# Performance work log

Measured on AMD Instinct MI355X. Metric: run time of the kernel, lower is better.

The kernel has to match this reference:

```python
import jax, jax.numpy as jnp
import numpy as np

A = 64            # n_agent == n_enemy == n_ally
MOVE = 4          # move_direction
ES = 5            # enemy_shape
ALS = 5           # ally_shape
NACT = 6          # n_actions
D = ES + ALS + NACT   # 16, transformer token dim
OBS = MOVE + ES * A + (ALS + NACT + A) * A  # 5124
B = 256


def setup_inputs() -> dict:
    key = jax.random.key(0)
    ks = jax.random.split(key, 5)
    s = 1.0 / np.sqrt(D)
    return {
        "inputs": jax.random.normal(ks[0], (B, A, OBS), dtype=jnp.float32),
        "Wq": jax.random.normal(ks[1], (D, D), dtype=jnp.float32) * s,
        "bq": jnp.zeros((D,), dtype=jnp.float32),
        "Wk": jax.random.normal(ks[2], (D, D), dtype=jnp.float32) * s,
        "bk": jnp.zeros((D,), dtype=jnp.float32),
        "Wv": jax.random.normal(ks[3], (D, D), dtype=jnp.float32) * s,
        "bv": jnp.zeros((D,), dtype=jnp.float32),
        "Wo": jax.random.normal(ks[4], (D, D), dtype=jnp.float32) * s,
        "bo": jnp.zeros((D,), dtype=jnp.float32),
    }


def reference(inputs, Wq, bq, Wk, bk, Wv, bv, Wo, bo):
    # dyn slice: skip move dirs, take enemy+ally blocks, reshape per agent,
    # keep first D=16 features of each agent row (drop the A-dim one-hot tail).
    dyn = inputs[:, :, MOVE: MOVE + ES * A + (ALS + NACT + A) * A]
    dyn = dyn.reshape(B, A, A, ES + ALS + NACT + A)[..., :D]  # [B, Ai, Atok, D]

    # single-head self-attention applied independently per (batch, agent i)
    q = dyn @ Wq + bq                                          # [B, Ai, Atok, D]
    k = dyn @ Wk + bk
    v = dyn @ Wv + bv
    scores = jnp.einsum('bitd,bisd->bits', q, k) / jnp.sqrt(jnp.float32(D))
    attn = jax.nn.softmax(scores, axis=-1)                      # [B, Ai, Atok, Atok]
    o = jnp.einsum('bits,bisd->bitd', attn, v) @ Wo + bo        # [B, Ai, Atok, D]

    # relu then sum over agent index i (the outer python loop's accumulation)
    x_sum = jax.nn.relu(o).sum(axis=1)                          # [B, Atok=A, D]

    return jnp.concatenate([inputs[:, :, :MOVE], x_sum], axis=2)  # [B, A, MOVE+D]
```

## Files before the change

kernel.cpp:

```cpp
#include <hip/hip_runtime.h>

#define NA 64
#define MOVE 4
#define OBS 5124
#define ROWS 80
#define NB 256
#define NTASK (NB * NA)
#define OUTC 20
#define WPB 8
#define NPART 8

#define WS_WQ 0
#define WS_WK 64
#define WS_WV 128
#define WS_BK 768
#define WS_BVO 784
#define WS_PART 1024

typedef __attribute__((ext_vector_type(8))) short bf16x8;
typedef __attribute__((ext_vector_type(4))) float f32x4;

__device__ __forceinline__ short f2bf(float f) {
    __bf16 h = (__bf16)f;
    return __builtin_bit_cast(short, h);
}
__device__ __forceinline__ bf16x8 mkfrag4(float a, float b, float c, float d) {
    bf16x8 t;
    t[0] = f2bf(a); t[1] = f2bf(b); t[2] = f2bf(c); t[3] = f2bf(d);
    t[4] = 0; t[5] = 0; t[6] = 0; t[7] = 0;
    return t;
}
__device__ __forceinline__ bf16x8 mkfrag8(f32x4 lo, f32x4 hi) {
    bf16x8 t;
    t[0] = f2bf(lo[0]); t[1] = f2bf(lo[1]); t[2] = f2bf(lo[2]); t[3] = f2bf(lo[3]);
    t[4] = f2bf(hi[0]); t[5] = f2bf(hi[1]); t[6] = f2bf(hi[2]); t[7] = f2bf(hi[3]);
    return t;
}

__global__ __launch_bounds__(256) void prep_kernel(
    const float* __restrict__ Wq,
    const float* __restrict__ Wk, const float* __restrict__ bk,
    const float* __restrict__ Wv, const float* __restrict__ bv,
    const float* __restrict__ Wo, const float* __restrict__ bo,
    float* __restrict__ ws)
{
    __shared__ float sWvo[256];
    const float SC = 0.36067376022224085f;
    int tid = threadIdx.x;
    {
        int e = tid >> 4, d = tid & 15;
        float acc = 0.f;
        #pragma unroll
        for (int c = 0; c < 16; ++c) acc += Wv[e * 16 + c] * Wo[c * 16 + d];
        sWvo[e * 16 + d] = acc;
    }
    __syncthreads();
    if (tid < 64) {
        int g = tid >> 4, c = tid & 15;
        bf16x8 q, k, v;
        #pragma unroll
        for (int r = 0; r < 4; ++r) {
            q[r] = f2bf(Wq[(4 * g + r) * 16 + c]);
            k[r] = f2bf(SC * Wk[(4 * g + r) * 16 + c]);
            v[r] = f2bf(sWvo[(4 * g + r) * 16 + c]);
        }
        #pragma unroll
        for (int r = 4; r < 8; ++r) { q[r] = 0; k[r] = 0; v[r] = 0; }
        ((bf16x8*)ws)[WS_WQ + tid] = q;
        ((bf16x8*)ws)[WS_WK + tid] = k;
        ((bf16x8*)ws)[WS_WV + tid] = v;
    }
    if (tid < 16) {
        ws[WS_BK + tid] = SC * bk[tid];
        float bb = bo[tid];
        #pragma unroll
        for (int c = 0; c < 16; ++c) bb += bv[c] * Wo[c * 16 + tid];
        ws[WS_BVO + tid] = bb;
    }
}

__global__ __launch_bounds__(512, 4) void attn_kernel(
    const float* __restrict__ inp,
    const float* __restrict__ bq,
    float* __restrict__ ws,
    float* __restrict__ out)
{
    __shared__ float sRed[WPB * 64 * OUTC];

    const int tid  = threadIdx.x;
    const int lane = tid & 63;
    const int w    = tid >> 6;
    const int idx  = blockIdx.x * WPB + w;
    const int g    = lane >> 4;
    const int c    = lane & 15;

    const bf16x8 wq = ((const bf16x8*)ws)[WS_WQ + lane];
    const bf16x8 wk = ((const bf16x8*)ws)[WS_WK + lane];
    const bf16x8 wv = ((const bf16x8*)ws)[WS_WV + lane];
    const float4 bq_r  = *(const float4*)(bq + 4 * g);
    const float4 bk_r  = *(const float4*)(ws + WS_BK + 4 * g);
    const float4 bvo_r = *(const float4*)(ws + WS_BVO + 4 * g);

    if (lane == 0) {
        float4 mv = *(const float4*)(inp + (size_t)idx * OBS);
        *(float4*)(out + (size_t)idx * OUTC) = mv;
    }

    const float* dynp = inp + (size_t)idx * OBS + MOVE;
    bf16x8 dy[4];
    #pragma unroll
    for (int i = 0; i < 4; ++i) {
        f32x4 f = __builtin_nontemporal_load(
            (const f32x4*)(dynp + (16 * i + c) * ROWS + 4 * g));
        dy[i] = mkfrag4(f[0], f[1], f[2], f[3]);
    }

    const f32x4 zc = {0.f, 0.f, 0.f, 0.f};

    bf16x8 qb[4], kb[4];
    f32x4 vC[4];
    #pragma unroll
    for (int i = 0; i < 4; ++i) {
        f32x4 qT = __builtin_amdgcn_mfma_f32_16x16x32_bf16(wq, dy[i], zc, 0, 0, 0);
        f32x4 kT = __builtin_amdgcn_mfma_f32_16x16x32_bf16(wk, dy[i], zc, 0, 0, 0);
        vC[i]    = __builtin_amdgcn_mfma_f32_16x16x32_bf16(dy[i], wv, zc, 0, 0, 0);
        qb[i] = mkfrag4(qT[0] + bq_r.x, qT[1] + bq_r.y, qT[2] + bq_r.z, qT[3] + bq_r.w);
        kb[i] = mkfrag4(kT[0] + bk_r.x, kT[1] + bk_r.y, kT[2] + bk_r.z, kT[3] + bk_r.w);
    }
    const bf16x8 vb_lo = mkfrag8(vC[0], vC[1]);
    const bf16x8 vb_hi = mkfrag8(vC[2], vC[3]);

    #pragma unroll
    for (int j = 0; j < 4; ++j) {
        f32x4 s0 = __builtin_amdgcn_mfma_f32_16x16x32_bf16(kb[0], qb[j], zc, 0, 0, 0);
        f32x4 s1 = __builtin_amdgcn_mfma_f32_16x16x32_bf16(kb[1], qb[j], zc, 0, 0, 0);
        f32x4 s2 = __builtin_amdgcn_mfma_f32_16x16x32_bf16(kb[2], qb[j], zc, 0, 0, 0);
        f32x4 s3 = __builtin_amdgcn_mfma_f32_16x16x32_bf16(kb[3], qb[j], zc, 0, 0, 0);

        float part = 0.f;
        #pragma unroll
        for (int r = 0; r < 4; ++r) {
            s0[r] = __builtin_amdgcn_exp2f(s0[r]); part += s0[r];
            s1[r] = __builtin_amdgcn_exp2f(s1[r]); part += s1[r];
            s2[r] = __builtin_amdgcn_exp2f(s2[r]); part += s2[r];
            s3[r] = __builtin_amdgcn_exp2f(s3[r]); part += s3[r];
        }
        part += __shfl_xor(part, 16);
        part += __shfl_xor(part, 32);
        float inv = __builtin_amdgcn_rcpf(part);

        bf16x8 p_lo = mkfrag8(s0, s1);
        bf16x8 p_hi = mkfrag8(s2, s3);

        f32x4 ot;
        ot = __builtin_amdgcn_mfma_f32_16x16x32_bf16(vb_lo, p_lo, zc, 0, 0, 0);
        ot = __builtin_amdgcn_mfma_f32_16x16x32_bf16(vb_hi, p_hi, ot, 0, 0, 0);

        float4 st;
        st.x = fmaxf(fmaf(ot[0], inv, bvo_r.x), 0.f);
        st.y = fmaxf(fmaf(ot[1], inv, bvo_r.y), 0.f);
        st.z = fmaxf(fmaf(ot[2], inv, bvo_r.z), 0.f);
        st.w = fmaxf(fmaf(ot[3], inv, bvo_r.w), 0.f);
        *(float4*)(&sRed[(w * 64 + 16 * j + c) * OUTC + 4 * g]) = st;
    }

    __syncthreads();

    if (tid < 256) {
        int t = tid >> 2, dq = tid & 3;
        float4 st = make_float4(0.f, 0.f, 0.f, 0.f);
        #pragma unroll
        for (int ww = 0; ww < WPB; ++ww) {
            const float4 a = *(const float4*)(&sRed[(ww * 64 + t) * OUTC + dq * 4]);
            st.x += a.x; st.y += a.y; st.z += a.z; st.w += a.w;
        }
        *(float4*)(ws + WS_PART + (size_t)blockIdx.x * 1024 + t * 16 + dq * 4) = st;
    }
}

__global__ __launch_bounds__(256) void reduce_kernel(
    const float* __restrict__ ws, float* __restrict__ out)
{
    const int b   = blockIdx.x;
    const int tid = threadIdx.x;
    const float* pb = ws + WS_PART + (size_t)b * (NPART * 1024);

    int e4 = tid * 4;
    float4 s = make_float4(0.f, 0.f, 0.f, 0.f);
    #pragma unroll
    for (int p = 0; p < NPART; ++p) {
        const float4 a = *(const float4*)(pb + p * 1024 + e4);
        s.x += a.x; s.y += a.y; s.z += a.z; s.w += a.w;
    }
    int t = e4 >> 4, d = e4 & 15;
    *(float4*)(out + ((size_t)b * NA + t) * OUTC + MOVE + d) = s;
}

extern "C" void kernel_launch(void* const* d_in, const int* in_sizes, int n_in,
                              void* d_out, int out_size, void* d_ws, size_t ws_size,
                              hipStream_t stream) {
    const float* inp = (const float*)d_in[0];
    const float* Wq  = (const float*)d_in[1];
    const float* bq  = (const float*)d_in[2];
    const float* Wk  = (const float*)d_in[3];
    const float* bk  = (const float*)d_in[4];
    const float* Wv  = (const float*)d_in[5];
    const float* bv  = (const float*)d_in[6];
    const float* Wo  = (const float*)d_in[7];
    const float* bo  = (const float*)d_in[8];
    float* out = (float*)d_out;
    float* ws  = (float*)d_ws;

    hipLaunchKernelGGL(prep_kernel, dim3(1), dim3(256), 0, stream, Wq, Wk, bk, Wv, bv, Wo, bo, ws);
    hipLaunchKernelGGL(attn_kernel, dim3(NTASK / WPB), dim3(512), 0, stream, inp, bq, ws, out);
    hipLaunchKernelGGL(reduce_kernel, dim3(NB), dim3(256), 0, stream, ws, out);
}
```

Before: 46.39 us.

## Fold Q/K biases into MFMA, stage dyn tile in LDS, shrink blocks to four waves

The Q and K biases are folded into the weight fragments through an extra constant-one column in the input fragment, so the per-element bias adds after each projection disappear. Each wave now loads its 64x16 input tile into shared memory and re-reads it for each projection, which shortens register live ranges, and the weight fragments are loaded only inside the scope where they are used. Blocks drop from 8 to 4 waves with a higher occupancy hint, which doubles the number of partial sums the reduce kernel must combine. This adds LDS traffic and more partial-sum writes in exchange for lower register pressure and higher occupancy.

```diff
diff --git a/kernel.cpp b/kernel.cpp
--- a/kernel.cpp
+++ b/kernel.cpp
@@ -7,13 +7,12 @@
 #define NB 256
 #define NTASK (NB * NA)
 #define OUTC 20
-#define WPB 8
-#define NPART 8
+#define WPB 4
+#define NPART 16
 
 #define WS_WQ 0
 #define WS_WK 64
 #define WS_WV 128
-#define WS_BK 768
 #define WS_BVO 784
 #define WS_PART 1024
 
@@ -24,21 +23,27 @@
     __bf16 h = (__bf16)f;
     return __builtin_bit_cast(short, h);
 }
-__device__ __forceinline__ bf16x8 mkfrag4(float a, float b, float c, float d) {
+__device__ __forceinline__ bf16x8 pack4(f32x4 v) {
     bf16x8 t;
-    t[0] = f2bf(a); t[1] = f2bf(b); t[2] = f2bf(c); t[3] = f2bf(d);
+    t[0] = f2bf(v[0]); t[1] = f2bf(v[1]); t[2] = f2bf(v[2]); t[3] = f2bf(v[3]);
     t[4] = 0; t[5] = 0; t[6] = 0; t[7] = 0;
     return t;
 }
-__device__ __forceinline__ bf16x8 mkfrag8(f32x4 lo, f32x4 hi) {
+__device__ __forceinline__ bf16x8 pack8(f32x4 lo, f32x4 hi) {
     bf16x8 t;
     t[0] = f2bf(lo[0]); t[1] = f2bf(lo[1]); t[2] = f2bf(lo[2]); t[3] = f2bf(lo[3]);
     t[4] = f2bf(hi[0]); t[5] = f2bf(hi[1]); t[6] = f2bf(hi[2]); t[7] = f2bf(hi[3]);
     return t;
 }
+__device__ __forceinline__ bf16x8 dyfrag(f32x4 v, short s4) {
+    bf16x8 t;
+    t[0] = f2bf(v[0]); t[1] = f2bf(v[1]); t[2] = f2bf(v[2]); t[3] = f2bf(v[3]);
+    t[4] = s4; t[5] = 0; t[6] = 0; t[7] = 0;
+    return t;
+}
 
 __global__ __launch_bounds__(256) void prep_kernel(
-    const float* __restrict__ Wq,
+    const float* __restrict__ Wq, const float* __restrict__ bq,
     const float* __restrict__ Wk, const float* __restrict__ bk,
     const float* __restrict__ Wv, const float* __restrict__ bv,
     const float* __restrict__ Wo, const float* __restrict__ bo,
@@ -63,15 +68,15 @@
             q[r] = f2bf(Wq[(4 * g + r) * 16 + c]);
             k[r] = f2bf(SC * Wk[(4 * g + r) * 16 + c]);
             v[r] = f2bf(sWvo[(4 * g + r) * 16 + c]);
-        }
-        #pragma unroll
-        for (int r = 4; r < 8; ++r) { q[r] = 0; k[r] = 0; v[r] = 0; }
+            q[4 + r] = (c == 0) ? f2bf(bq[4 * g + r]) : (short)0;
+            k[4 + r] = (c == 0) ? f2bf(SC * bk[4 * g + r]) : (short)0;
+            v[4 + r] = 0;
+        }
         ((bf16x8*)ws)[WS_WQ + tid] = q;
         ((bf16x8*)ws)[WS_WK + tid] = k;
         ((bf16x8*)ws)[WS_WV + tid] = v;
     }
     if (tid < 16) {
-        ws[WS_BK + tid] = SC * bk[tid];
         float bb = bo[tid];
         #pragma unroll
         for (int c = 0; c < 16; ++c) bb += bv[c] * Wo[c * 16 + tid];
@@ -79,13 +84,12 @@
     }
 }
 
-__global__ __launch_bounds__(512, 4) void attn_kernel(
+__global__ __launch_bounds__(256, 8) void attn_kernel(
     const float* __restrict__ inp,
-    const float* __restrict__ bq,
-    float* __restrict__ ws,
+    const float* __restrict__ ws,
     float* __restrict__ out)
 {
-    __shared__ float sRed[WPB * 64 * OUTC];
+    __shared__ float sBuf[WPB * 1024];
 
     const int tid  = threadIdx.x;
     const int lane = tid & 63;
@@ -93,64 +97,90 @@
     const int idx  = blockIdx.x * WPB + w;
     const int g    = lane >> 4;
     const int c    = lane & 15;
-
-    const bf16x8 wq = ((const bf16x8*)ws)[WS_WQ + lane];
-    const bf16x8 wk = ((const bf16x8*)ws)[WS_WK + lane];
-    const bf16x8 wv = ((const bf16x8*)ws)[WS_WV + lane];
-    const float4 bq_r  = *(const float4*)(bq + 4 * g);
-    const float4 bk_r  = *(const float4*)(ws + WS_BK + 4 * g);
-    const float4 bvo_r = *(const float4*)(ws + WS_BVO + 4 * g);
+    float* chunk = sBuf + (w << 10);
 
     if (lane == 0) {
         float4 mv = *(const float4*)(inp + (size_t)idx * OBS);
         *(float4*)(out + (size_t)idx * OUTC) = mv;
     }
 
-    const float* dynp = inp + (size_t)idx * OBS + MOVE;
-    bf16x8 dy[4];
-    #pragma unroll
-    for (int i = 0; i < 4; ++i) {
-        f32x4 f = __builtin_nontemporal_load(
-            (const f32x4*)(dynp + (16 * i + c) * ROWS + 4 * g));
-        dy[i] = mkfrag4(f[0], f[1], f[2], f[3]);
+    {
+        const float* dynp = inp + (size_t)idx * OBS + MOVE + (size_t)c * ROWS + 4 * g;
+        f32x4 t0 = *(const f32x4*)(dynp + 0 * 16 * ROWS);
+        f32x4 t1 = *(const f32x4*)(dynp + 1 * 16 * ROWS);
+        f32x4 t2 = *(const f32x4*)(dynp + 2 * 16 * ROWS);
+        f32x4 t3 = *(const f32x4*)(dynp + 3 * 16 * ROWS);
+        *(f32x4*)(chunk + (16 * 0 + c) * 16 + 4 * g) = t0;
+        *(f32x4*)(chunk + (16 * 1 + c) * 16 + 4 * g) = t1;
+        *(f32x4*)(chunk + (16 * 2 + c) * 16 + 4 * g) = t2;
+        *(f32x4*)(chunk + (16 * 3 + c) * 16 + 4 * g) = t3;
     }
 
     const f32x4 zc = {0.f, 0.f, 0.f, 0.f};
-
-    bf16x8 qb[4], kb[4];
-    f32x4 vC[4];
-    #pragma unroll
-    for (int i = 0; i < 4; ++i) {
-        f32x4 qT = __builtin_amdgcn_mfma_f32_16x16x32_bf16(wq, dy[i], zc, 0, 0, 0);
-        f32x4 kT = __builtin_amdgcn_mfma_f32_16x16x32_bf16(wk, dy[i], zc, 0, 0, 0);
-        vC[i]    = __builtin_amdgcn_mfma_f32_16x16x32_bf16(dy[i], wv, zc, 0, 0, 0);
-        qb[i] = mkfrag4(qT[0] + bq_r.x, qT[1] + bq_r.y, qT[2] + bq_r.z, qT[3] + bq_r.w);
-        kb[i] = mkfrag4(kT[0] + bk_r.x, kT[1] + bk_r.y, kT[2] + bk_r.z, kT[3] + bk_r.w);
-    }
-    const bf16x8 vb_lo = mkfrag8(vC[0], vC[1]);
-    const bf16x8 vb_hi = mkfrag8(vC[2], vC[3]);
+    const short s4 = (g == 0) ? (short)0x3f80 : (short)0;
+    const float4 bvo_r = *(const float4*)(ws + WS_BVO + 4 * g);
+
+    bf16x8 qb[4], kb[4], vb_lo, vb_hi;
+    {
+        const bf16x8 wq = ((const bf16x8*)ws)[WS_WQ + lane];
+        #pragma unroll
+        for (int i = 0; i < 4; ++i) {
+            f32x4 d = *(const f32x4*)(chunk + i * 256 + c * 16 + 4 * g);
+            qb[i] = pack4(__builtin_amdgcn_mfma_f32_16x16x32_bf16(wq, dyfrag(d, s4), zc, 0, 0, 0));
+        }
+    }
+    {
+        const bf16x8 wk = ((const bf16x8*)ws)[WS_WK + lane];
+        #pragma unroll
+        for (int i = 0; i < 4; ++i) {
+            f32x4 d = *(const f32x4*)(chunk + i * 256 + c * 16 + 4 * g);
+            kb[i] = pack4(__builtin_amdgcn_mfma_f32_16x16x32_bf16(wk, dyfrag(d, s4), zc, 0, 0, 0));
+        }
+    }
+    {
+        const bf16x8 wv = ((const bf16x8*)ws)[WS_WV + lane];
+        f32x4 v0, v1, v2, v3;
+        {
+            f32x4 d = *(const f32x4*)(chunk + 0 * 256 + c * 16 + 4 * g);
+            v0 = __builtin_amdgcn_mfma_f32_16x16x32_bf16(dyfrag(d, s4), wv, zc, 0, 0, 0);
+            d = *(const f32x4*)(chunk + 1 * 256 + c * 16 + 4 * g);
+            v1 = __builtin_amdgcn_mfma_f32_16x16x32_bf16(dyfrag(d, s4), wv, zc, 0, 0, 0);
+            d = *(const f32x4*)(chunk + 2 * 256 + c * 16 + 4 * g);
+            v2 = __builtin_amdgcn_mfma_f32_16x16x32_bf16(dyfrag(d, s4), wv, zc, 0, 0, 0);
+            d = *(const f32x4*)(chunk + 3 * 256 + c * 16 + 4 * g);
+            v3 = __builtin_amdgcn_mfma_f32_16x16x32_bf16(dyfrag(d, s4), wv, zc, 0, 0, 0);
+        }
+        vb_lo = pack8(v0, v1);
+        vb_hi = pack8(v2, v3);
+    }
 
     #pragma unroll
     for (int j = 0; j < 4; ++j) {
-        f32x4 s0 = __builtin_amdgcn_mfma_f32_16x16x32_bf16(kb[0], qb[j], zc, 0, 0, 0);
-        f32x4 s1 = __builtin_amdgcn_mfma_f32_16x16x32_bf16(kb[1], qb[j], zc, 0, 0, 0);
-        f32x4 s2 = __builtin_amdgcn_mfma_f32_16x16x32_bf16(kb[2], qb[j], zc, 0, 0, 0);
-        f32x4 s3 = __builtin_amdgcn_mfma_f32_16x16x32_bf16(kb[3], qb[j], zc, 0, 0, 0);
-
         float part = 0.f;
-        #pragma unroll
-        for (int r = 0; r < 4; ++r) {
-            s0[r] = __builtin_amdgcn_exp2f(s0[r]); part += s0[r];
-            s1[r] = __builtin_amdgcn_exp2f(s1[r]); part += s1[r];
-            s2[r] = __builtin_amdgcn_exp2f(s2[r]); part += s2[r];
-            s3[r] = __builtin_amdgcn_exp2f(s3[r]); part += s3[r];
+        bf16x8 p_lo, p_hi;
+        {
+            f32x4 s0 = __builtin_amdgcn_mfma_f32_16x16x32_bf16(kb[0], qb[j], zc, 0, 0, 0);
+            f32x4 s1 = __builtin_amdgcn_mfma_f32_16x16x32_bf16(kb[1], qb[j], zc, 0, 0, 0);
+            #pragma unroll
+            for (int r = 0; r < 4; ++r) {
+                s0[r] = __builtin_amdgcn_exp2f(s0[r]); part += s0[r];
+                s1[r] = __builtin_amdgcn_exp2f(s1[r]); part += s1[r];
+            }
+            p_lo = pack8(s0, s1);
+        }
+        {
+            f32x4 s2 = __builtin_amdgcn_mfma_f32_16x16x32_bf16(kb[2], qb[j], zc, 0, 0, 0);
+            f32x4 s3 = __builtin_amdgcn_mfma_f32_16x16x32_bf16(kb[3], qb[j], zc, 0, 0, 0);
+            #pragma unroll
+            for (int r = 0; r < 4; ++r) {
+                s2[r] = __builtin_amdgcn_exp2f(s2[r]); part += s2[r];
+                s3[r] = __builtin_amdgcn_exp2f(s3[r]); part += s3[r];
+            }
+            p_hi = pack8(s2, s3);
         }
         part += __shfl_xor(part, 16);
         part += __shfl_xor(part, 32);
         float inv = __builtin_amdgcn_rcpf(part);
-
-        bf16x8 p_lo = mkfrag8(s0, s1);
-        bf16x8 p_hi = mkfrag8(s2, s3);
 
         f32x4 ot;
         ot = __builtin_amdgcn_mfma_f32_16x16x32_bf16(vb_lo, p_lo, zc, 0, 0, 0);
@@ -161,20 +191,20 @@
         st.y = fmaxf(fmaf(ot[1], inv, bvo_r.y), 0.f);
         st.z = fmaxf(fmaf(ot[2], inv, bvo_r.z), 0.f);
         st.w = fmaxf(fmaf(ot[3], inv, bvo_r.w), 0.f);
-        *(float4*)(&sRed[(w * 64 + 16 * j + c) * OUTC + 4 * g]) = st;
+        *(float4*)(chunk + (16 * j + c) * 16 + 4 * g) = st;
     }
 
     __syncthreads();
 
-    if (tid < 256) {
+    {
         int t = tid >> 2, dq = tid & 3;
         float4 st = make_float4(0.f, 0.f, 0.f, 0.f);
         #pragma unroll
         for (int ww = 0; ww < WPB; ++ww) {
-            const float4 a = *(const float4*)(&sRed[(ww * 64 + t) * OUTC + dq * 4]);
+            const float4 a = *(const float4*)(&sBuf[(ww << 10) + t * 16 + dq * 4]);
             st.x += a.x; st.y += a.y; st.z += a.z; st.w += a.w;
         }
-        *(float4*)(ws + WS_PART + (size_t)blockIdx.x * 1024 + t * 16 + dq * 4) = st;
+        *(float4*)((float*)ws + WS_PART + (size_t)blockIdx.x * 1024 + t * 16 + dq * 4) = st;
     }
 }
 
@@ -211,7 +241,8 @@
     float* out = (float*)d_out;
     float* ws  = (float*)d_ws;
 
-    hipLaunchKernelGGL(prep_kernel, dim3(1), dim3(256), 0, stream, Wq, Wk, bk, Wv, bv, Wo, bo, ws);
-    hipLaunchKernelGGL(attn_kernel, dim3(NTASK / WPB), dim3(512), 0, stream, inp, bq, ws, out);
+    hipLaunchKernelGGL(prep_kernel, dim3(1), dim3(256), 0, stream,
+                       Wq, bq, Wk, bk, Wv, bv, Wo, bo, ws);
+    hipLaunchKernelGGL(attn_kernel, dim3(NTASK / WPB), dim3(256), 0, stream, inp, ws, out);
     hipLaunchKernelGGL(reduce_kernel, dim3(NB), dim3(256), 0, stream, ws, out);
 }
```

Result: slower. 50.10 us (+8.0%).
